# Kernel optimization log

Hardware: AMD Instinct MI355X
Metric: run time of the kernel (lower is better)

The kernel has to match this reference:

```python
import jax, jax.numpy as jnp
import numpy as np

N = 100_000   # nodes
E = 1_600_000 # edges
F = 32        # input features
G = 512       # graphs in batch
EPS = 1e-5    # batchnorm eps


def setup_inputs() -> dict:
    key = jax.random.key(0)
    ks = jax.random.split(key, 24)
    d = {
        "x": jax.random.normal(ks[0], (N, F), jnp.float32),
        "edge_index": jax.random.randint(ks[1], (2, E), 0, N),
        "batch": jnp.sort(jax.random.randint(ks[2], (N,), 0, G)),
        "Wl1": jax.random.normal(ks[3], (30, F), jnp.float32) * 0.1,
        "bl1": jax.random.normal(ks[4], (30,), jnp.float32) * 0.1,
        "Wr1": jax.random.normal(ks[5], (30, F), jnp.float32) * 0.1,
        "Wl2": jax.random.normal(ks[6], (30, 30), jnp.float32) * 0.1,
        "bl2": jax.random.normal(ks[7], (30,), jnp.float32) * 0.1,
        "Wr2": jax.random.normal(ks[8], (30, 30), jnp.float32) * 0.1,
        "g1": jax.random.uniform(ks[9], (30,), jnp.float32) + 0.5,
        "b1": jax.random.normal(ks[10], (30,), jnp.float32) * 0.1,
        "m1": jax.random.normal(ks[11], (30,), jnp.float32) * 0.1,
        "v1": jax.random.uniform(ks[12], (30,), jnp.float32) + 0.5,
        "g2": jax.random.uniform(ks[13], (30,), jnp.float32) + 0.5,
        "b2": jax.random.normal(ks[14], (30,), jnp.float32) * 0.1,
        "m2": jax.random.normal(ks[15], (30,), jnp.float32) * 0.1,
        "v2": jax.random.uniform(ks[16], (30,), jnp.float32) + 0.5,
        "W1": jax.random.normal(ks[17], (10, 60), jnp.float32) * 0.1,
        "bb1": jax.random.normal(ks[18], (10,), jnp.float32) * 0.1,
        "W2": jax.random.normal(ks[19], (1, 10), jnp.float32) * 0.1,
        "bb2": jax.random.normal(ks[20], (1,), jnp.float32) * 0.1,
    }
    return d


def reference(x, edge_index, batch, Wl1, bl1, Wr1, Wl2, bl2, Wr2,
              g1, b1, m1, v1, g2, b2, m2, v2, W1, bb1, W2, bb2):
    src, dst = edge_index[0], edge_index[1]

    def sage(h, Wl, bl, Wr):
        # mean aggregation of source features into targets (PyG SAGEConv default)
        s = jax.ops.segment_sum(h[src], dst, num_segments=N)
        cnt = jax.ops.segment_sum(jnp.ones((E,), h.dtype), dst, num_segments=N)
        agg = s / jnp.maximum(cnt, 1.0)[:, None]
        return agg @ Wl.T + bl + h @ Wr.T

    def bn(h, g, b, m, v):  # BatchNorm1d, eval mode (running stats)
        return (h - m) * jax.lax.rsqrt(v + EPS) * g + b

    h = bn(jax.nn.relu(sage(x, Wl1, bl1, Wr1)), g1, b1, m1, v1)
    h = bn(jax.nn.relu(sage(h, Wl2, bl2, Wr2)), g2, b2, m2, v2)

    # dual segment pooling over graphs
    xmax = jax.ops.segment_max(h, batch, num_segments=G)
    xmax = jnp.where(jnp.isfinite(xmax), xmax, 0.0)  # empty graphs -> 0
    s = jax.ops.segment_sum(h, batch, num_segments=G)
    c = jax.ops.segment_sum(jnp.ones((N,), h.dtype), batch, num_segments=G)
    xmean = s / jnp.maximum(c, 1.0)[:, None]

    z = jnp.concatenate([xmax, xmean], axis=1)  # [G, 60]
    z = jax.nn.relu(z @ W1.T + bb1)
    z = z @ W2.T + bb2
    return jax.nn.sigmoid(z)  # [G, 1]
```

## Files before the change

### kernel.cpp

```cpp
#include <hip/hip_runtime.h>
#include <hip/hip_fp16.h>

#define NN 100000
#define NE 1600000
#define FI 32
#define FH 30
#define PAD 32
#define NG 512
#define NBK 782
#define BNODES 128
#define SCB 2048
#define CBLK 32
#define NCHUNK (SCB / CBLK)
#define CAP 4096
#define NB1 391
#define F8B 3125

__global__ __launch_bounds__(256) void k_phist(const int* __restrict__ dst,
                                               unsigned short* __restrict__ partial,
                                               const float* __restrict__ x, unsigned* __restrict__ x8)
{
    __shared__ int cnt[NBK];
    if (blockIdx.x >= SCB) {
        int i = (blockIdx.x - SCB) * 256 + threadIdx.x;
        if (i < NN * 8) {
            float4 f = ((const float4*)x)[i];
            unsigned w = 0;
            w = __builtin_amdgcn_cvt_pk_fp8_f32(f.x, f.y, w, false);
            w = __builtin_amdgcn_cvt_pk_fp8_f32(f.z, f.w, w, true);
            x8[i] = w;
        }
        return;
    }
    for (int i = threadIdx.x; i < NBK; i += 256) cnt[i] = 0;
    __syncthreads();
    for (int e2 = blockIdx.x * 256 + threadIdx.x; e2 < NE / 2; e2 += SCB * 256) {
        int2 d2 = ((const int2*)dst)[e2];
        atomicAdd(&cnt[d2.x >> 7], 1);
        atomicAdd(&cnt[d2.y >> 7], 1);
    }
    __syncthreads();
    for (int i = threadIdx.x; i < NBK; i += 256)
        partial[(size_t)blockIdx.x * NBK + i] = (unsigned short)cnt[i];
}

__global__ __launch_bounds__(256) void k_csum(const unsigned short* __restrict__ partial,
                                              int* __restrict__ chunksum)
{
    int t = blockIdx.x * 256 + threadIdx.x;
    if (t >= NCHUNK * NBK) return;
    int c = t / NBK, b = t - c * NBK;
    int s = 0;
    #pragma unroll 8
    for (int k = 0; k < CBLK; ++k)
        s += partial[(size_t)(c * CBLK + k) * NBK + b];
    chunksum[c * NBK + b] = s;
}

__global__ __launch_bounds__(1024) void k_cscan(const int* __restrict__ chunksum,
                                                int* __restrict__ chunkbase, int* __restrict__ bktOff)
{
    __shared__ int tmp[1024];
    int tid = threadIdx.x;
    int total = 0;
    if (tid < NBK) {
        for (int c = 0; c < NCHUNK; ++c) total += chunksum[c * NBK + tid];
    }
    tmp[tid] = (tid < NBK) ? total : 0;
    __syncthreads();
    for (int off = 1; off < 1024; off <<= 1) {
        int t = (tid >= off) ? tmp[tid - off] : 0;
        __syncthreads();
        tmp[tid] += t;
        __syncthreads();
    }
    if (tid < NBK) {
        bktOff[tid] = tmp[tid] - total;
        int run = 0;
        for (int c = 0; c < NCHUNK; ++c) {
            chunkbase[c * NBK + tid] = run;
            run += chunksum[c * NBK + tid];
        }
    }
    if (tid == 0) bktOff[NBK] = NE;
}

__global__ __launch_bounds__(256) void k_base(unsigned short* __restrict__ partial,
                                              const int* __restrict__ chunkbase)
{
    int t = blockIdx.x * 256 + threadIdx.x;
    if (t >= NCHUNK * NBK) return;
    int c = t / NBK, b = t - c * NBK;
    int run = chunkbase[c * NBK + b];
    #pragma unroll 8
    for (int k = 0; k < CBLK; ++k) {
        size_t idx = (size_t)(c * CBLK + k) * NBK + b;
        int v = partial[idx];
        partial[idx] = (unsigned short)run;
        run += v;
    }
}

__global__ __launch_bounds__(256) void k_bscat(const int* __restrict__ src, const int* __restrict__ dst,
                                               const unsigned short* __restrict__ partial,
                                               const int* __restrict__ bktOff,
                                               unsigned* __restrict__ pairs)
{
    __shared__ int sbase[NBK];
    __shared__ int scnt[NBK];
    for (int i = threadIdx.x; i < NBK; i += 256) {
        sbase[i] = bktOff[i] + (int)partial[(size_t)blockIdx.x * NBK + i];
        scnt[i] = 0;
    }
    __syncthreads();
    for (int e2 = blockIdx.x * 256 + threadIdx.x; e2 < NE / 2; e2 += SCB * 256) {
        int2 s2 = ((const int2*)src)[e2];
        int2 d2 = ((const int2*)dst)[e2];
        int b0 = d2.x >> 7;
        int r0 = atomicAdd(&scnt[b0], 1);
        pairs[sbase[b0] + r0] = ((unsigned)s2.x << 7) | (unsigned)(d2.x & 127);
        int b1 = d2.y >> 7;
        int r1 = atomicAdd(&scnt[b1], 1);
        pairs[sbase[b1] + r1] = ((unsigned)s2.y << 7) | (unsigned)(d2.y & 127);
    }
}

__global__ __launch_bounds__(256) void k_csr(
    const int* __restrict__ bktOff, const unsigned* __restrict__ pairs,
    int* __restrict__ rowstart, int* __restrict__ col)
{
    __shared__ unsigned sp[CAP];
    __shared__ int bins[BNODES], binpos[BNODES], stmp[BNODES];
    int tid = threadIdx.x;
    int bkt = blockIdx.x;
    int gbase = bktOff[bkt];
    int cnt = bktOff[bkt + 1] - gbase;
    if (tid < BNODES) bins[tid] = 0;
    __syncthreads();
    bool inl = (cnt <= CAP);
    if (inl) {
        for (int i = tid; i < cnt; i += 256) {
            unsigned u = pairs[gbase + i];
            sp[i] = u;
            atomicAdd(&bins[u & 127], 1);
        }
    } else {
        for (int i = tid; i < cnt; i += 256)
            atomicAdd(&bins[pairs[gbase + i] & 127], 1);
    }
    __syncthreads();
    if (tid < BNODES) stmp[tid] = bins[tid];
    __syncthreads();
    for (int off = 1; off < BNODES; off <<= 1) {
        int t = 0;
        if (tid < BNODES && tid >= off) t = stmp[tid - off];
        __syncthreads();
        if (tid < BNODES) stmp[tid] += t;
        __syncthreads();
    }
    if (tid < BNODES) {
        int ex = stmp[tid] - bins[tid];
        binpos[tid] = ex;
        int n = (bkt << 7) + tid;
        if (n < NN) rowstart[n] = gbase + ex;
        if (bkt == 0 && tid == 0) rowstart[NN] = NE;
    }
    __syncthreads();
    if (inl) {
        for (int i = tid; i < cnt; i += 256) {
            unsigned u = sp[i];
            int p = atomicAdd(&binpos[u & 127], 1);
            col[gbase + p] = (int)(u >> 7);
        }
    } else {
        for (int i = tid; i < cnt; i += 256) {
            unsigned u = pairs[gbase + i];
            int p = atomicAdd(&binpos[u & 127], 1);
            col[gbase + p] = (int)(u >> 7);
        }
    }
}

__global__ __launch_bounds__(256) void k_agg8(const int* __restrict__ rowstart,
                                              const int* __restrict__ col,
                                              const unsigned* __restrict__ hin,
                                              __half2* __restrict__ aggh)
{
    int tid = blockIdx.x * 256 + threadIdx.x;
    int n = tid >> 6;
    if (n >= NN) return;
    int lane = threadIdx.x & 63;
    int q = lane & 7;
    int grp = lane >> 3;
    int rs = rowstart[n], re = rowstart[n + 1];
    float a0 = 0.0f, a1 = 0.0f, a2 = 0.0f, a3 = 0.0f;
    for (int e = rs + grp; e < re; e += 8) {
        unsigned u = hin[(size_t)col[e] * 8 + q];
        auto lo = __builtin_amdgcn_cvt_pk_f32_fp8(u, false);
        auto hi = __builtin_amdgcn_cvt_pk_f32_fp8(u, true);
        a0 += lo[0]; a1 += lo[1]; a2 += hi[0]; a3 += hi[1];
    }
    #pragma unroll
    for (int off = 8; off < 64; off <<= 1) {
        a0 += __shfl_xor(a0, off); a1 += __shfl_xor(a1, off);
        a2 += __shfl_xor(a2, off); a3 += __shfl_xor(a3, off);
    }
    if (lane < 8) {
        float inv = (re > rs) ? 1.0f / (float)(re - rs) : 0.0f;
        union { __half2 h[2]; uint2 u; } pk;
        pk.h[0] = __floats2half2_rn(a0 * inv, a1 * inv);
        pk.h[1] = __floats2half2_rn(a2 * inv, a3 * inv);
        ((uint2*)(aggh + (size_t)n * 16))[q] = pk.u;
    }
}

__global__ __launch_bounds__(256) void k_t1(
    const float* __restrict__ x, const __half2* __restrict__ aggh,
    const float* __restrict__ Wl, const float* __restrict__ bl, const float* __restrict__ Wr,
    const float* __restrict__ g, const float* __restrict__ b,
    const float* __restrict__ m, const float* __restrict__ v,
    unsigned* __restrict__ h1_8)
{
    __shared__ float sWl[FH * FI], sWr[FH * FI], sBias[FH], sScale[FH], sShift[FH];
    for (int i = threadIdx.x; i < FH * FI; i += 256) { sWl[i] = Wl[i]; sWr[i] = Wr[i]; }
    if (threadIdx.x < FH) {
        int j = threadIdx.x;
        float sc = g[j] * rsqrtf(v[j] + 1e-5f);
        sBias[j] = bl[j];
        sScale[j] = sc;
        sShift[j] = b[j] - m[j] * sc;
    }
    __syncthreads();
    int n = blockIdx.x * 256 + threadIdx.x;
    if (n >= NN) return;
    float xr[FI], ar[FI];
    #pragma unroll
    for (int k = 0; k < FI; k += 4) {
        float4 xv = *(const float4*)(x + (size_t)n * FI + k);
        xr[k] = xv.x; xr[k+1] = xv.y; xr[k+2] = xv.z; xr[k+3] = xv.w;
    }
    const __half2* arow = aggh + (size_t)n * 16;
    #pragma unroll
    for (int k2 = 0; k2 < 16; ++k2) {
        float2 fv = __half22float2(arow[k2]);
        ar[2 * k2] = fv.x; ar[2 * k2 + 1] = fv.y;
    }
    float res[32];
    for (int j = 0; j < FH; ++j) {
        float acc = sBias[j];
        #pragma unroll
        for (int k = 0; k < FI; ++k)
            acc += ar[k] * sWl[j * FI + k] + xr[k] * sWr[j * FI + k];
        acc = fmaxf(acc, 0.0f);
        res[j] = acc * sScale[j] + sShift[j];
    }
    res[30] = 0.0f; res[31] = 0.0f;
    unsigned* row = h1_8 + (size_t)n * 8;
    #pragma unroll
    for (int w = 0; w < 8; ++w) {
        unsigned pw = 0;
        pw = __builtin_amdgcn_cvt_pk_fp8_f32(res[4*w],   res[4*w+1], pw, false);
        pw = __builtin_amdgcn_cvt_pk_fp8_f32(res[4*w+2], res[4*w+3], pw, true);
        row[w] = pw;
    }
}

__global__ __launch_bounds__(256) void k_t2(
    const unsigned* __restrict__ h1_8, const __half2* __restrict__ aggh,
    const float* __restrict__ Wl, const float* __restrict__ bl, const float* __restrict__ Wr,
    const float* __restrict__ g, const float* __restrict__ b,
    const float* __restrict__ m, const float* __restrict__ v,
    __half2* __restrict__ h2h)
{
    __shared__ float sWl[FH * FH], sWr[FH * FH], sBias[FH], sScale[FH], sShift[FH];
    for (int i = threadIdx.x; i < FH * FH; i += 256) { sWl[i] = Wl[i]; sWr[i] = Wr[i]; }
    if (threadIdx.x < FH) {
        int j = threadIdx.x;
        float sc = g[j] * rsqrtf(v[j] + 1e-5f);
        sBias[j] = bl[j];
        sScale[j] = sc;
        sShift[j] = b[j] - m[j] * sc;
    }
    __syncthreads();
    int n = blockIdx.x * 256 + threadIdx.x;
    if (n >= NN) return;
    float xr[32], ar[FH];
    const unsigned* hrow = h1_8 + (size_t)n * 8;
    #pragma unroll
    for (int w = 0; w < 8; ++w) {
        unsigned u = hrow[w];
        auto lo = __builtin_amdgcn_cvt_pk_f32_fp8(u, false);
        auto hi = __builtin_amdgcn_cvt_pk_f32_fp8(u, true);
        xr[4*w] = lo[0]; xr[4*w+1] = lo[1]; xr[4*w+2] = hi[0]; xr[4*w+3] = hi[1];
    }
    const __half2* arow = aggh + (size_t)n * 16;
    #pragma unroll
    for (int k2 = 0; k2 < FH / 2; ++k2) {
        float2 fv = __half22float2(arow[k2]);
        ar[2 * k2] = fv.x; ar[2 * k2 + 1] = fv.y;
    }
    float res[FH];
    for (int j = 0; j < FH; ++j) {
        float acc = sBias[j];
        #pragma unroll
        for (int k = 0; k < FH; ++k)
            acc += ar[k] * sWl[j * FH + k] + xr[k] * sWr[j * FH + k];
        acc = fmaxf(acc, 0.0f);
        res[j] = acc * sScale[j] + sShift[j];
    }
    __half2* row = h2h + (size_t)n * (PAD / 2);
    #pragma unroll
    for (int j = 0; j < FH; j += 2)
        row[j >> 1] = __floats2half2_rn(res[j], res[j + 1]);
}

__global__ __launch_bounds__(256) void k_pool(
    const __half* __restrict__ h2, const int* __restrict__ batch,
    const float* __restrict__ W1, const float* __restrict__ bb1,
    const float* __restrict__ W2, const float* __restrict__ bb2,
    float* __restrict__ out)
{
    __shared__ float sS[8][FH], sM[8][FH], sz[2 * FH], st[10];
    int tid = threadIdx.x;
    int gi = blockIdx.x;
    int lo = 0, hi = NN;
    while (lo < hi) { int mid = (lo + hi) >> 1; if (batch[mid] < gi) lo = mid + 1; else hi = mid; }
    int start = lo;
    hi = NN;
    while (lo < hi) { int mid = (lo + hi) >> 1; if (batch[mid] <= gi) lo = mid + 1; else hi = mid; }
    int end = lo;

    int f = tid & 31;
    int ng = tid >> 5;
    float sum = 0.0f, mx = -INFINITY;
    if (f < FH) {
        for (int n = start + ng; n < end; n += 8) {
            float val = __half2float(h2[(size_t)n * PAD + f]);
            sum += val;
            mx = fmaxf(mx, val);
        }
        sS[ng][f] = sum;
        sM[ng][f] = mx;
    }
    __syncthreads();
    if (tid < FH) {
        float s = 0.0f, mm = -INFINITY;
        #pragma unroll
        for (int w = 0; w < 8; ++w) { s += sS[w][tid]; mm = fmaxf(mm, sM[w][tid]); }
        int c = end - start;
        sz[tid]      = (c > 0) ? mm : 0.0f;
        sz[FH + tid] = (c > 0) ? s / (float)c : 0.0f;
    }
    __syncthreads();
    if (tid < 10) {
        float t = bb1[tid];
        for (int k = 0; k < 2 * FH; ++k) t += sz[k] * W1[tid * 2 * FH + k];
        st[tid] = fmaxf(t, 0.0f);
    }
    __syncthreads();
    if (tid == 0) {
        float o = bb2[0];
        for (int j = 0; j < 10; ++j) o += st[j] * W2[j];
        out[gi] = 1.0f / (1.0f + expf(-o));
    }
}

extern "C" void kernel_launch(void* const* d_in, const int* in_sizes, int n_in,
                              void* d_out, int out_size, void* d_ws, size_t ws_size,
                              hipStream_t stream)
{
    const float* x   = (const float*)d_in[0];
    const int*   ei  = (const int*)d_in[1];
    const int*   bat = (const int*)d_in[2];
    const float* Wl1 = (const float*)d_in[3];
    const float* bl1 = (const float*)d_in[4];
    const float* Wr1 = (const float*)d_in[5];
    const float* Wl2 = (const float*)d_in[6];
    const float* bl2 = (const float*)d_in[7];
    const float* Wr2 = (const float*)d_in[8];
    const float* g1  = (const float*)d_in[9];
    const float* b1  = (const float*)d_in[10];
    const float* m1  = (const float*)d_in[11];
    const float* v1  = (const float*)d_in[12];
    const float* g2  = (const float*)d_in[13];
    const float* b2  = (const float*)d_in[14];
    const float* m2  = (const float*)d_in[15];
    const float* v2  = (const float*)d_in[16];
    const float* W1  = (const float*)d_in[17];
    const float* bb1 = (const float*)d_in[18];
    const float* W2  = (const float*)d_in[19];
    const float* bb2 = (const float*)d_in[20];

    const int* src = ei;
    const int* dst = ei + NE;

    unsigned short* partial = (unsigned short*)d_ws;
    int* chunksum  = (int*)((char*)d_ws + (size_t)SCB * NBK * 2);
    int* chunkbase = chunksum + NCHUNK * NBK;
    int* bktOff    = chunkbase + NCHUNK * NBK;
    int* rowstart  = bktOff + NBK + 2;
    unsigned* pairs = (unsigned*)(rowstart + NN + 4);
    int* col       = (int*)(pairs + NE);
    unsigned* x8   = (unsigned*)(col + NE);
    unsigned* h1_8 = x8 + (size_t)NN * 8;
    __half2*  aggh = (__half2*)(h1_8 + (size_t)NN * 8);
    __half2*  h2h  = aggh + (size_t)NN * 16;

    int pb = (NCHUNK * NBK + 255) / 256;

    k_phist<<<SCB + F8B, 256, 0, stream>>>(dst, partial, x, x8);
    k_csum <<<pb, 256, 0, stream>>>(partial, chunksum);
    k_cscan<<<1, 1024, 0, stream>>>(chunksum, chunkbase, bktOff);
    k_base <<<pb, 256, 0, stream>>>(partial, chunkbase);
    k_bscat<<<SCB, 256, 0, stream>>>(src, dst, partial, bktOff, pairs);
    k_csr  <<<NBK, 256, 0, stream>>>(bktOff, pairs, rowstart, col);

    int ab = (NN * 64 + 255) / 256;
    k_agg8<<<ab, 256, 0, stream>>>(rowstart, col, x8, aggh);
    k_t1<<<NB1, 256, 0, stream>>>(x, aggh, Wl1, bl1, Wr1, g1, b1, m1, v1, h1_8);
    k_agg8<<<ab, 256, 0, stream>>>(rowstart, col, h1_8, aggh);
    k_t2<<<NB1, 256, 0, stream>>>(h1_8, aggh, Wl2, bl2, Wr2, g2, b2, m2, v2, h2h);
    k_pool<<<NG, 256, 0, stream>>>((const __half*)h2h, bat, W1, bb1, W2, bb2, (float*)d_out);
}
```

Measured before the change: 181.6 us.

## Fuse neighbor aggregation with SAGE linear transform into persistent per-layer kernel

```diff
diff --git a/kernel.cpp b/kernel.cpp
--- a/kernel.cpp
+++ b/kernel.cpp
@@ -13,8 +13,8 @@
 #define CBLK 32
 #define NCHUNK (SCB / CBLK)
 #define CAP 4096
-#define NB1 391
 #define F8B 3125
+#define LGB 2048
 
 __global__ __launch_bounds__(256) void k_phist(const int* __restrict__ dst,
                                                unsigned short* __restrict__ partial,
@@ -181,137 +181,98 @@
     }
 }
 
-__global__ __launch_bounds__(256) void k_agg8(const int* __restrict__ rowstart,
-                                              const int* __restrict__ col,
-                                              const unsigned* __restrict__ hin,
-                                              __half2* __restrict__ aggh)
-{
-    int tid = blockIdx.x * 256 + threadIdx.x;
-    int n = tid >> 6;
-    if (n >= NN) return;
-    int lane = threadIdx.x & 63;
+template<bool OUT8>
+__global__ __launch_bounds__(256) void k_layer(
+    const int* __restrict__ rowstart, const int* __restrict__ col,
+    const unsigned* __restrict__ hin,
+    const float* __restrict__ Wl, const float* __restrict__ bl, const float* __restrict__ Wr,
+    int K,
+    const float* __restrict__ g, const float* __restrict__ b,
+    const float* __restrict__ m, const float* __restrict__ v,
+    unsigned* __restrict__ out8, __half2* __restrict__ outh)
+{
+    __shared__ float sWl[32 * 33], sWr[32 * 33];
+    __shared__ float sBias[32], sScale[32], sShift[32];
+    int tid = threadIdx.x;
+    for (int i = tid; i < 32 * 32; i += 256) {
+        int j = i >> 5, k = i & 31;
+        bool real = (j < FH) && (k < K);
+        sWl[j * 33 + k] = real ? Wl[j * K + k] : 0.0f;
+        sWr[j * 33 + k] = real ? Wr[j * K + k] : 0.0f;
+    }
+    if (tid < 32) {
+        if (tid < FH) {
+            float sc = g[tid] * rsqrtf(v[tid] + 1e-5f);
+            sBias[tid] = bl[tid];
+            sScale[tid] = sc;
+            sShift[tid] = b[tid] - m[tid] * sc;
+        } else {
+            sBias[tid] = 0.0f; sScale[tid] = 0.0f; sShift[tid] = 0.0f;
+        }
+    }
+    __syncthreads();
+
+    int lane = tid & 63;
     int q = lane & 7;
     int grp = lane >> 3;
-    int rs = rowstart[n], re = rowstart[n + 1];
-    float a0 = 0.0f, a1 = 0.0f, a2 = 0.0f, a3 = 0.0f;
-    for (int e = rs + grp; e < re; e += 8) {
-        unsigned u = hin[(size_t)col[e] * 8 + q];
-        auto lo = __builtin_amdgcn_cvt_pk_f32_fp8(u, false);
-        auto hi = __builtin_amdgcn_cvt_pk_f32_fp8(u, true);
-        a0 += lo[0]; a1 += lo[1]; a2 += hi[0]; a3 += hi[1];
-    }
-    #pragma unroll
-    for (int off = 8; off < 64; off <<= 1) {
-        a0 += __shfl_xor(a0, off); a1 += __shfl_xor(a1, off);
-        a2 += __shfl_xor(a2, off); a3 += __shfl_xor(a3, off);
-    }
-    if (lane < 8) {
+    int gwid = (blockIdx.x * 256 + tid) >> 6;
+    int nwaves = LGB * 4;
+
+    for (int n = gwid; n < NN; n += nwaves) {
+        int rs = rowstart[n], re = rowstart[n + 1];
+        float a0 = 0.0f, a1 = 0.0f, a2 = 0.0f, a3 = 0.0f;
+        for (int e = rs + grp; e < re; e += 8) {
+            unsigned u = hin[(size_t)col[e] * 8 + q];
+            auto lo = __builtin_amdgcn_cvt_pk_f32_fp8(u, false);
+            auto hi = __builtin_amdgcn_cvt_pk_f32_fp8(u, true);
+            a0 += lo[0]; a1 += lo[1]; a2 += hi[0]; a3 += hi[1];
+        }
+        #pragma unroll
+        for (int off = 8; off < 64; off <<= 1) {
+            a0 += __shfl_xor(a0, off); a1 += __shfl_xor(a1, off);
+            a2 += __shfl_xor(a2, off); a3 += __shfl_xor(a3, off);
+        }
         float inv = (re > rs) ? 1.0f / (float)(re - rs) : 0.0f;
-        union { __half2 h[2]; uint2 u; } pk;
-        pk.h[0] = __floats2half2_rn(a0 * inv, a1 * inv);
-        pk.h[1] = __floats2half2_rn(a2 * inv, a3 * inv);
-        ((uint2*)(aggh + (size_t)n * 16))[q] = pk.u;
-    }
-}
-
-__global__ __launch_bounds__(256) void k_t1(
-    const float* __restrict__ x, const __half2* __restrict__ aggh,
-    const float* __restrict__ Wl, const float* __restrict__ bl, const float* __restrict__ Wr,
-    const float* __restrict__ g, const float* __restrict__ b,
-    const float* __restrict__ m, const float* __restrict__ v,
-    unsigned* __restrict__ h1_8)
-{
-    __shared__ float sWl[FH * FI], sWr[FH * FI], sBias[FH], sScale[FH], sShift[FH];
-    for (int i = threadIdx.x; i < FH * FI; i += 256) { sWl[i] = Wl[i]; sWr[i] = Wr[i]; }
-    if (threadIdx.x < FH) {
-        int j = threadIdx.x;
-        float sc = g[j] * rsqrtf(v[j] + 1e-5f);
-        sBias[j] = bl[j];
-        sScale[j] = sc;
-        sShift[j] = b[j] - m[j] * sc;
-    }
-    __syncthreads();
-    int n = blockIdx.x * 256 + threadIdx.x;
-    if (n >= NN) return;
-    float xr[FI], ar[FI];
-    #pragma unroll
-    for (int k = 0; k < FI; k += 4) {
-        float4 xv = *(const float4*)(x + (size_t)n * FI + k);
-        xr[k] = xv.x; xr[k+1] = xv.y; xr[k+2] = xv.z; xr[k+3] = xv.w;
-    }
-    const __half2* arow = aggh + (size_t)n * 16;
-    #pragma unroll
-    for (int k2 = 0; k2 < 16; ++k2) {
-        float2 fv = __half22float2(arow[k2]);
-        ar[2 * k2] = fv.x; ar[2 * k2 + 1] = fv.y;
-    }
-    float res[32];
-    for (int j = 0; j < FH; ++j) {
-        float acc = sBias[j];
+        a0 *= inv; a1 *= inv; a2 *= inv; a3 *= inv;
+        unsigned su = hin[(size_t)n * 8 + q];
+        auto slo = __builtin_amdgcn_cvt_pk_f32_fp8(su, false);
+        auto shi = __builtin_amdgcn_cvt_pk_f32_fp8(su, true);
+        float s0 = slo[0], s1 = slo[1], s2 = shi[0], s3 = shi[1];
+
+        int k0 = q * 4;
         #pragma unroll
-        for (int k = 0; k < FI; ++k)
-            acc += ar[k] * sWl[j * FI + k] + xr[k] * sWr[j * FI + k];
-        acc = fmaxf(acc, 0.0f);
-        res[j] = acc * sScale[j] + sShift[j];
-    }
-    res[30] = 0.0f; res[31] = 0.0f;
-    unsigned* row = h1_8 + (size_t)n * 8;
-    #pragma unroll
-    for (int w = 0; w < 8; ++w) {
-        unsigned pw = 0;
-        pw = __builtin_amdgcn_cvt_pk_fp8_f32(res[4*w],   res[4*w+1], pw, false);
-        pw = __builtin_amdgcn_cvt_pk_fp8_f32(res[4*w+2], res[4*w+3], pw, true);
-        row[w] = pw;
-    }
-}
-
-__global__ __launch_bounds__(256) void k_t2(
-    const unsigned* __restrict__ h1_8, const __half2* __restrict__ aggh,
-    const float* __restrict__ Wl, const float* __restrict__ bl, const float* __restrict__ Wr,
-    const float* __restrict__ g, const float* __restrict__ b,
-    const float* __restrict__ m, const float* __restrict__ v,
-    __half2* __restrict__ h2h)
-{
-    __shared__ float sWl[FH * FH], sWr[FH * FH], sBias[FH], sScale[FH], sShift[FH];
-    for (int i = threadIdx.x; i < FH * FH; i += 256) { sWl[i] = Wl[i]; sWr[i] = Wr[i]; }
-    if (threadIdx.x < FH) {
-        int j = threadIdx.x;
-        float sc = g[j] * rsqrtf(v[j] + 1e-5f);
-        sBias[j] = bl[j];
-        sScale[j] = sc;
-        sShift[j] = b[j] - m[j] * sc;
-    }
-    __syncthreads();
-    int n = blockIdx.x * 256 + threadIdx.x;
-    if (n >= NN) return;
-    float xr[32], ar[FH];
-    const unsigned* hrow = h1_8 + (size_t)n * 8;
-    #pragma unroll
-    for (int w = 0; w < 8; ++w) {
-        unsigned u = hrow[w];
-        auto lo = __builtin_amdgcn_cvt_pk_f32_fp8(u, false);
-        auto hi = __builtin_amdgcn_cvt_pk_f32_fp8(u, true);
-        xr[4*w] = lo[0]; xr[4*w+1] = lo[1]; xr[4*w+2] = hi[0]; xr[4*w+3] = hi[1];
-    }
-    const __half2* arow = aggh + (size_t)n * 16;
-    #pragma unroll
-    for (int k2 = 0; k2 < FH / 2; ++k2) {
-        float2 fv = __half22float2(arow[k2]);
-        ar[2 * k2] = fv.x; ar[2 * k2 + 1] = fv.y;
-    }
-    float res[FH];
-    for (int j = 0; j < FH; ++j) {
-        float acc = sBias[j];
-        #pragma unroll
-        for (int k = 0; k < FH; ++k)
-            acc += ar[k] * sWl[j * FH + k] + xr[k] * sWr[j * FH + k];
-        acc = fmaxf(acc, 0.0f);
-        res[j] = acc * sScale[j] + sShift[j];
-    }
-    __half2* row = h2h + (size_t)n * (PAD / 2);
-    #pragma unroll
-    for (int j = 0; j < FH; j += 2)
-        row[j >> 1] = __floats2half2_rn(res[j], res[j + 1]);
+        for (int p = 0; p < 4; ++p) {
+            int j = p * 8 + grp;
+            const float* wl = &sWl[j * 33 + k0];
+            const float* wr = &sWr[j * 33 + k0];
+            float part = a0 * wl[0] + a1 * wl[1] + a2 * wl[2] + a3 * wl[3]
+                       + s0 * wr[0] + s1 * wr[1] + s2 * wr[2] + s3 * wr[3];
+            part += __shfl_xor(part, 1);
+            part += __shfl_xor(part, 2);
+            part += __shfl_xor(part, 4);
+            float acc = fmaxf(part + sBias[j], 0.0f);
+            float resp = acc * sScale[j] + sShift[j];
+            if (OUT8) {
+                int srcA = (lane & 1) ? 32 : 0;
+                float v0 = __shfl(resp, srcA);
+                float v1 = __shfl(resp, srcA + 8);
+                float v2 = __shfl(resp, srcA + 16);
+                float v3 = __shfl(resp, srcA + 24);
+                if (lane < 2) {
+                    unsigned pw = 0;
+                    pw = __builtin_amdgcn_cvt_pk_fp8_f32(v0, v1, pw, false);
+                    pw = __builtin_amdgcn_cvt_pk_fp8_f32(v2, v3, pw, true);
+                    out8[(size_t)n * 8 + 2 * p + lane] = pw;
+                }
+            } else {
+                int i = lane & 3;
+                float f0 = __shfl(resp, 16 * i);
+                float f1 = __shfl(resp, 16 * i + 8);
+                if (lane < 4)
+                    outh[(size_t)n * 16 + 4 * p + i] = __floats2half2_rn(f0, f1);
+            }
+        }
+    }
 }
 
 __global__ __launch_bounds__(256) void k_pool(
@@ -403,8 +364,7 @@
     int* col       = (int*)(pairs + NE);
     unsigned* x8   = (unsigned*)(col + NE);
     unsigned* h1_8 = x8 + (size_t)NN * 8;
-    __half2*  aggh = (__half2*)(h1_8 + (size_t)NN * 8);
-    __half2*  h2h  = aggh + (size_t)NN * 16;
+    __half2*  h2h  = (__half2*)(h1_8 + (size_t)NN * 8);
 
     int pb = (NCHUNK * NBK + 255) / 256;
 
@@ -415,10 +375,9 @@
     k_bscat<<<SCB, 256, 0, stream>>>(src, dst, partial, bktOff, pairs);
     k_csr  <<<NBK, 256, 0, stream>>>(bktOff, pairs, rowstart, col);
 
-    int ab = (NN * 64 + 255) / 256;
-    k_agg8<<<ab, 256, 0, stream>>>(rowstart, col, x8, aggh);
-    k_t1<<<NB1, 256, 0, stream>>>(x, aggh, Wl1, bl1, Wr1, g1, b1, m1, v1, h1_8);
-    k_agg8<<<ab, 256, 0, stream>>>(rowstart, col, h1_8, aggh);
-    k_t2<<<NB1, 256, 0, stream>>>(h1_8, aggh, Wl2, bl2, Wr2, g2, b2, m2, v2, h2h);
+    k_layer<true> <<<LGB, 256, 0, stream>>>(rowstart, col, x8,
+                                            Wl1, bl1, Wr1, FI, g1, b1, m1, v1, h1_8, nullptr);
+    k_layer<false><<<LGB, 256, 0, stream>>>(rowstart, col, h1_8,
+                                            Wl2, bl2, Wr2, FH, g2, b2, m2, v2, nullptr, h2h);
     k_pool<<<NG, 256, 0, stream>>>((const __half*)h2h, bat, W1, bb1, W2, bb2, (float*)d_out);
 }
```

Result: slower. 212.5 us (+17.0%).
